# Performance work log

Hardware: AMD Instinct MI355X
Metric: run time of the kernel (lower is better)

The kernel has to match this reference:

```python
import jax, jax.numpy as jnp
import numpy as np

SEG_LENS = [2048, 8192]
DIL_RATES = [1, 2]


def _dilated_attention(q, k, v, is_causal):
    # q,k,v: [b, n, h, d]
    b, n, h, d = q.shape
    ng = len(SEG_LENS)
    g = h // ng  # heads per group (even split)
    scale = 1.0 / np.sqrt(d).astype(np.float32)
    out = jnp.zeros_like(q)
    for i, (s, r) in enumerate(zip(SEG_LENS, DIL_RATES)):
        hs = i * g
        offset = i % r  # offset_idx % dilation_rate, as in _create_dilation_pattern
        idx = np.arange(offset, s, r)  # dilated positions within a segment, length m
        m = idx.shape[0]
        ns = n // s  # number of segments
        # reshape to segments then gather dilated positions: [b, ns, m, g, d]
        qg = q[:, :, hs:hs + g, :].reshape(b, ns, s, g, d)[:, :, idx]
        kg = k[:, :, hs:hs + g, :].reshape(b, ns, s, g, d)[:, :, idx]
        vg = v[:, :, hs:hs + g, :].reshape(b, ns, s, g, d)[:, :, idx]
        # segment-local attention over dilated tokens only (structured sparsity)
        scores = jnp.einsum('bsqhd,bskhd->bshqk', qg, kg) * scale
        if is_causal:
            cm = np.tril(np.ones((m, m), dtype=bool))  # idx is sorted -> causal in dilated order
            scores = jnp.where(cm, scores, -jnp.inf)
        attn = jax.nn.softmax(scores, axis=-1)
        og = jnp.einsum('bshqk,bskhd->bsqhd', attn, vg)  # [b, ns, m, g, d]
        # scatter back to full segment positions; non-dilated positions stay zero
        full = jnp.zeros((b, ns, s, g, d), q.dtype).at[:, :, idx].set(og)
        out = out.at[:, :, hs:hs + g, :].set(full.reshape(b, n, g, d))
    return out


def setup_inputs() -> dict:
    key = jax.random.key(0)
    k1, k2, k3 = jax.random.split(key, 3)
    shape = (1, 8192, 8, 64)
    q = jax.random.normal(k1, shape, dtype=jnp.float32)
    k = jax.random.normal(k2, shape, dtype=jnp.float32)
    v = jax.random.normal(k3, shape, dtype=jnp.float32)
    return {"q": q, "k": k, "v": v, "is_causal": 1}


def reference(q, k, v, is_causal):
    return _dilated_attention(q, k, v, bool(is_causal))
```

## Files before the change

kernel.cpp:

```cpp
#include <hip/hip_runtime.h>


#define LP 72

typedef __attribute__((ext_vector_type(8))) short bf16x8;
typedef __attribute__((ext_vector_type(4))) float f32x4;
typedef const unsigned int __attribute__((address_space(1)))* gp1;
typedef unsigned int __attribute__((address_space(3)))* lp3;

__device__ __forceinline__ unsigned short f2bf(float f) {
  unsigned u = __builtin_bit_cast(unsigned, f);
  u += 0x7fff + ((u >> 16) & 1);
  return (unsigned short)(u >> 16);
}

__device__ __forceinline__ int region_base(int head) {
  return (head < 4) ? head * 524288 : 2097152 + (head - 4) * 262144;
}

__device__ __forceinline__ void gl_lds16(const unsigned short* g, unsigned short* l) {
  __builtin_amdgcn_global_load_lds((gp1)g, (lp3)l, 16, 0, 0);
}

__global__ __launch_bounds__(256, 4)
void prep_kernel(const float* __restrict__ K, const float* __restrict__ V,
                 unsigned short* __restrict__ Kb, unsigned short* __restrict__ Vt) {
  __shared__ unsigned short sT[64][LP];
  const int bid = blockIdx.x;
  int head, pos0, rate, off;
  if (bid < 512) { head = bid >> 7; pos0 = (bid & 127) * 64; rate = 1; off = 0; }
  else { int b = bid - 512; head = 4 + (b >> 6); pos0 = (b & 63) * 64; rate = 2; off = 1; }
  const int rb = region_base(head);
  const int tid = threadIdx.x;
  const int row = tid >> 2, dg = tid & 3;
  const long tok = (long)(pos0 + row) * rate + off;

  {
    const float* kp = K + tok * 512 + head * 64 + dg * 16;
    unsigned short tmp[16];
    #pragma unroll
    for (int i = 0; i < 4; ++i) {
      float4 f = ((const float4*)kp)[i];
      tmp[i * 4 + 0] = f2bf(f.x); tmp[i * 4 + 1] = f2bf(f.y);
      tmp[i * 4 + 2] = f2bf(f.z); tmp[i * 4 + 3] = f2bf(f.w);
    }
    const int s = row & 7;
    unsigned short* dstrow = Kb + rb + (long)(pos0 + row) * 64;
    *(int4*)(dstrow + (((2 * dg)     ^ s) * 8)) = ((int4*)tmp)[0];
    *(int4*)(dstrow + (((2 * dg + 1) ^ s) * 8)) = ((int4*)tmp)[1];
  }

  {
    const float* vp = V + tok * 512 + head * 64 + dg * 16;
    #pragma unroll
    for (int i = 0; i < 4; ++i) {
      float4 f = ((const float4*)vp)[i];
      unsigned* p = (unsigned*)&sT[row][dg * 16 + i * 4];
      p[0] = (unsigned)f2bf(f.x) | ((unsigned)f2bf(f.y) << 16);
      p[1] = (unsigned)f2bf(f.z) | ((unsigned)f2bf(f.w) << 16);
    }
  }
  __syncthreads();

  {
    const int wv = tid >> 6, lane = tid & 63;
    unsigned pk[8];
    #pragma unroll
    for (int j = 0; j < 8; ++j) {
      unsigned lo = sT[wv * 16 + 2 * j][lane];
      unsigned hi = sT[wv * 16 + 2 * j + 1][lane];
      pk[j] = lo | (hi << 16);
    }
    const int s = lane & 7;
    unsigned short* dstrow = Vt + rb + (long)pos0 * 64 + lane * 64;
    int4 a = {(int)pk[0], (int)pk[1], (int)pk[2], (int)pk[3]};
    int4 b = {(int)pk[4], (int)pk[5], (int)pk[6], (int)pk[7]};
    *(int4*)(dstrow + (((2 * wv)     ^ s) * 8)) = a;
    *(int4*)(dstrow + (((2 * wv + 1) ^ s) * 8)) = b;
  }
}

__global__ __launch_bounds__(256, 2)
void attn_kernel(const float* __restrict__ Q, const unsigned short* __restrict__ Kb,
                 const unsigned short* __restrict__ Vt, const int* __restrict__ IC,
                 float* __restrict__ O, float* __restrict__ Slots) {
  __shared__ __attribute__((aligned(16))) unsigned short sK[2][4096];
  __shared__ __attribute__((aligned(16))) unsigned short sV[2][4096];
  __shared__ __attribute__((aligned(16))) unsigned short sP[4][1024];

  const int bid = blockIdx.x;
  int head, q0, seg0, mseg, rate, off, grp, chunk, slot;
  if (bid < 512) {
    int h4 = bid & 3;
    int u = bid >> 2;
    chunk = u >> 6;
    int t = 63 - (u & 63);
    head = 4 + h4; seg0 = 0; mseg = 4096;
    rate = 2; off = 1; grp = 1;
    q0 = t * 64;
    slot = (h4 * 64 + t) * 2 + chunk;
  } else {
    int cc = bid - 512;
    int job = (cc & 7) | ((cc >> 8) << 3);
    int tloc = (cc & 255) >> 3;
    head = job & 3;
    seg0 = (job >> 2) * 2048;
    q0 = seg0 + tloc * 64; mseg = 2048;
    rate = 1; off = 0; grp = 0; chunk = 0; slot = 0;
  }
  const int rb = region_base(head);
  const bool causal = (*IC) != 0;
  const int tid = threadIdx.x, wave = tid >> 6, lane = tid & 63;
  const int l16 = lane & 15, quad = lane >> 4;
  const int ch0 = ((quad ^ (l16 & 7)) * 8);
  const int ch1 = ch0 ^ 32;

  const int qloc = q0 - seg0;
  const int diagkb = qloc >> 6;
  const int nkb = causal ? diagkb + 1 : (mseg >> 6);
  const int klo = grp ? chunk * 32 : 0;
  const int khi = grp ? min(nkb, klo + 32) : nkb;
  if (klo >= khi) return;

  const float QSCALE = 0.18033688011112042f;
  bf16x8 aQ[2];
  {
    long tok = (long)(q0 + wave * 16 + l16) * rate + off;
    const float* qp = Q + tok * 512 + head * 64 + quad * 8;
    #pragma unroll
    for (int kc = 0; kc < 2; ++kc) {
      float4 f0 = ((const float4*)(qp + kc * 32))[0];
      float4 f1 = ((const float4*)(qp + kc * 32))[1];
      bf16x8 a;
      a[0] = (short)f2bf(f0.x * QSCALE); a[1] = (short)f2bf(f0.y * QSCALE);
      a[2] = (short)f2bf(f0.z * QSCALE); a[3] = (short)f2bf(f0.w * QSCALE);
      a[4] = (short)f2bf(f1.x * QSCALE); a[5] = (short)f2bf(f1.y * QSCALE);
      a[6] = (short)f2bf(f1.z * QSCALE); a[7] = (short)f2bf(f1.w * QSCALE);
      aQ[kc] = a;
    }
  }

  f32x4 oacc[4], lacc;
  lacc = (f32x4){0.f, 0.f, 0.f, 0.f};
  #pragma unroll
  for (int dt = 0; dt < 4; ++dt) oacc[dt] = (f32x4){0.f, 0.f, 0.f, 0.f};
  bf16x8 vones;
  #pragma unroll
  for (int i = 0; i < 8; ++i) vones[i] = (short)0x3F80;

  unsigned short* myP = &sP[wave][0];
  const unsigned short* Ksrc = Kb + rb + (long)seg0 * 64;
  const unsigned short* Vsrc = Vt + rb + (long)seg0 * 64;

  const int o0 = wave * 1024;
  const int lo = lane * 8;
  {
    const unsigned short* kt = Ksrc + (long)klo * 4096;
    const unsigned short* vt = Vsrc + (long)klo * 4096;
    gl_lds16(kt + o0 + lo,       &sK[0][o0]);
    gl_lds16(kt + o0 + 512 + lo, &sK[0][o0 + 512]);
    gl_lds16(vt + o0 + lo,       &sV[0][o0]);
    gl_lds16(vt + o0 + 512 + lo, &sV[0][o0 + 512]);
  }

  for (int kb = klo; kb < khi; ++kb) {
    const int cur = (kb - klo) & 1;
    __syncthreads();
    if (kb + 1 < khi) {
      const unsigned short* kt = Ksrc + (long)(kb + 1) * 4096;
      const unsigned short* vt = Vsrc + (long)(kb + 1) * 4096;
      gl_lds16(kt + o0 + lo,       &sK[cur ^ 1][o0]);
      gl_lds16(kt + o0 + 512 + lo, &sK[cur ^ 1][o0 + 512]);
      gl_lds16(vt + o0 + lo,       &sV[cur ^ 1][o0]);
      gl_lds16(vt + o0 + 512 + lo, &sV[cur ^ 1][o0 + 512]);
    }
    const unsigned short* kbuf = &sK[cur][0];
    const unsigned short* vbuf = &sV[cur][0];

    f32x4 sc[4];
    #pragma unroll
    for (int c = 0; c < 4; ++c) {
      const unsigned short* krow = &kbuf[(c * 16 + l16) * 64];
      bf16x8 b0 = *(const bf16x8*)(krow + ch0);
      bf16x8 b1 = *(const bf16x8*)(krow + ch1);
      f32x4 z = (f32x4){0.f, 0.f, 0.f, 0.f};
      z = __builtin_amdgcn_mfma_f32_16x16x32_bf16(aQ[0], b0, z, 0, 0, 0);
      z = __builtin_amdgcn_mfma_f32_16x16x32_bf16(aQ[1], b1, z, 0, 0, 0);
      sc[c] = z;
    }

    const bool needMask = causal && (kb == diagkb);
    #pragma unroll
    for (int c = 0; c < 4; ++c) {
      #pragma unroll
      for (int r = 0; r < 4; ++r) {
        float e = __builtin_amdgcn_exp2f(sc[c][r]);
        if (needMask && (kb * 64 + c * 16 + l16 > qloc + wave * 16 + quad * 4 + r)) e = 0.f;
        const int qrow = quad * 4 + r;
        const int cidx = c * 2 + (l16 >> 3);
        myP[qrow * 64 + ((cidx ^ (qrow & 7)) << 3) + (l16 & 7)] = f2bf(e);
      }
    }
    const int swr = l16 & 7;
    bf16x8 aP0 = *(const bf16x8*)&myP[l16 * 64 + ((quad ^ swr) << 3)];
    bf16x8 aP1 = *(const bf16x8*)&myP[l16 * 64 + (((quad + 4) ^ swr) << 3)];
    lacc = __builtin_amdgcn_mfma_f32_16x16x32_bf16(aP0, vones, lacc, 0, 0, 0);
    lacc = __builtin_amdgcn_mfma_f32_16x16x32_bf16(aP1, vones, lacc, 0, 0, 0);

    #pragma unroll
    for (int dt = 0; dt < 4; ++dt) {
      const unsigned short* vrow = &vbuf[(dt * 16 + l16) * 64];
      bf16x8 v0 = *(const bf16x8*)(vrow + ch0);
      bf16x8 v1 = *(const bf16x8*)(vrow + ch1);
      oacc[dt] = __builtin_amdgcn_mfma_f32_16x16x32_bf16(aP0, v0, oacc[dt], 0, 0, 0);
      oacc[dt] = __builtin_amdgcn_mfma_f32_16x16x32_bf16(aP1, v1, oacc[dt], 0, 0, 0);
    }
  }

  if (grp == 1) {
    float* S = Slots + (long)slot * 4160;
    #pragma unroll
    for (int r = 0; r < 4; ++r) {
      int row = wave * 16 + quad * 4 + r;
      #pragma unroll
      for (int dt = 0; dt < 4; ++dt)
        S[row * 64 + dt * 16 + l16] = oacc[dt][r];
    }
    if (l16 == 0) {
      #pragma unroll
      for (int r = 0; r < 4; ++r)
        S[4096 + wave * 16 + quad * 4 + r] = lacc[r];
    }
  } else {
    #pragma unroll
    for (int r = 0; r < 4; ++r) {
      int tq = q0 + wave * 16 + quad * 4 + r;
      long tok = (long)tq * rate + off;
      float inv = 1.0f / lacc[r];
      float* dst = O + tok * 512 + head * 64 + l16;
      #pragma unroll
      for (int dt = 0; dt < 4; ++dt)
        dst[dt * 16] = oacc[dt][r] * inv;
    }
  }
}

__global__ __launch_bounds__(256, 4)
void combine_kernel(const float* __restrict__ Slots, const int* __restrict__ IC,
                    float* __restrict__ O) {
  const int b = blockIdx.x;
  const int h4 = b >> 6, t = b & 63;
  const bool causal = (*IC) != 0;
  const int nkb = causal ? t + 1 : 64;
  const int nc = (nkb > 32) ? 2 : 1;
  const float* s0 = Slots + (long)((h4 * 64 + t) * 2) * 4160;
  const int tid = threadIdx.x;
  const int row = tid >> 2, dq = (tid & 3) * 16;

  float4 acc[4];
  const float4* p0 = (const float4*)(s0 + row * 64 + dq);
  #pragma unroll
  for (int i = 0; i < 4; ++i) acc[i] = p0[i];
  float l = s0[4096 + row];
  if (nc == 2) {
    const float* s1 = s0 + 4160;
    const float4* p1 = (const float4*)(s1 + row * 64 + dq);
    #pragma unroll
    for (int i = 0; i < 4; ++i) {
      float4 v = p1[i];
      acc[i].x += v.x; acc[i].y += v.y; acc[i].z += v.z; acc[i].w += v.w;
    }
    l += s1[4096 + row];
  }
  const float inv = 1.0f / l;
  const long tok = (long)(t * 64 + row) * 2 + 1;
  float* dst = O + tok * 512 + (4 + h4) * 64 + dq;
  #pragma unroll
  for (int i = 0; i < 4; ++i) {
    float4 o = {acc[i].x * inv, acc[i].y * inv, acc[i].z * inv, acc[i].w * inv};
    ((float4*)dst)[i] = o;
  }
  float* dste = O + (tok - 1) * 512 + (4 + h4) * 64 + dq;
  const float4 z = {0.f, 0.f, 0.f, 0.f};
  #pragma unroll
  for (int i = 0; i < 4; ++i) ((float4*)dste)[i] = z;
}

extern "C" void kernel_launch(void* const* d_in, const int* in_sizes, int n_in,
                              void* d_out, int out_size, void* d_ws, size_t ws_size,
                              hipStream_t stream) {
  const float* q = (const float*)d_in[0];
  const float* k = (const float*)d_in[1];
  const float* v = (const float*)d_in[2];
  const int* ic = (const int*)d_in[3];
  unsigned short* Kb = (unsigned short*)d_ws;
  unsigned short* Vt = Kb + 3145728;
  float* Slots = (float*)((char*)d_ws + 12582912);
  prep_kernel<<<dim3(768), dim3(256), 0, stream>>>(k, v, Kb, Vt);
  attn_kernel<<<dim3(1024), dim3(256), 0, stream>>>(q, Kb, Vt, ic, (float*)d_out, Slots);
  combine_kernel<<<dim3(256), dim3(256), 0, stream>>>(Slots, ic, (float*)d_out);
}
```

Baseline: 138.8 us.

## Transpose MFMA operand roles to compute S^T and O^T, drop ones-MFMA row sum

Swaps the A/B operands of the QK and PV MFMAs so each lane holds a full query column, which lets the softmax denominator be a per-lane scalar sum plus two cross-lane shuffles instead of an extra pair of MFMAs against a ones vector. P is written to LDS as packed 64-bit stores instead of scalar 16-bit stores. Output and partial slots are written as float4 vectors instead of scalar floats. The row sum is now taken in fp32 before bf16 rounding, which changes numerics slightly.

```diff
diff --git a/kernel.cpp b/kernel.cpp
--- a/kernel.cpp
+++ b/kernel.cpp
@@ -123,7 +123,7 @@
   if (klo >= khi) return;
 
   const float QSCALE = 0.18033688011112042f;
-  bf16x8 aQ[2];
+  bf16x8 bQ[2];
   {
     long tok = (long)(q0 + wave * 16 + l16) * rate + off;
     const float* qp = Q + tok * 512 + head * 64 + quad * 8;
@@ -136,17 +136,14 @@
       a[2] = (short)f2bf(f0.z * QSCALE); a[3] = (short)f2bf(f0.w * QSCALE);
       a[4] = (short)f2bf(f1.x * QSCALE); a[5] = (short)f2bf(f1.y * QSCALE);
       a[6] = (short)f2bf(f1.z * QSCALE); a[7] = (short)f2bf(f1.w * QSCALE);
-      aQ[kc] = a;
-    }
-  }
-
-  f32x4 oacc[4], lacc;
-  lacc = (f32x4){0.f, 0.f, 0.f, 0.f};
+      bQ[kc] = a;
+    }
+  }
+
+  f32x4 oacc[4];
+  float lsum = 0.f;
   #pragma unroll
   for (int dt = 0; dt < 4; ++dt) oacc[dt] = (f32x4){0.f, 0.f, 0.f, 0.f};
-  bf16x8 vones;
-  #pragma unroll
-  for (int i = 0; i < 8; ++i) vones[i] = (short)0x3F80;
 
   unsigned short* myP = &sP[wave][0];
   const unsigned short* Ksrc = Kb + rb + (long)seg0 * 64;
@@ -181,66 +178,66 @@
     #pragma unroll
     for (int c = 0; c < 4; ++c) {
       const unsigned short* krow = &kbuf[(c * 16 + l16) * 64];
-      bf16x8 b0 = *(const bf16x8*)(krow + ch0);
-      bf16x8 b1 = *(const bf16x8*)(krow + ch1);
+      bf16x8 a0 = *(const bf16x8*)(krow + ch0);
+      bf16x8 a1 = *(const bf16x8*)(krow + ch1);
       f32x4 z = (f32x4){0.f, 0.f, 0.f, 0.f};
-      z = __builtin_amdgcn_mfma_f32_16x16x32_bf16(aQ[0], b0, z, 0, 0, 0);
-      z = __builtin_amdgcn_mfma_f32_16x16x32_bf16(aQ[1], b1, z, 0, 0, 0);
+      z = __builtin_amdgcn_mfma_f32_16x16x32_bf16(a0, bQ[0], z, 0, 0, 0);
+      z = __builtin_amdgcn_mfma_f32_16x16x32_bf16(a1, bQ[1], z, 0, 0, 0);
       sc[c] = z;
     }
 
     const bool needMask = causal && (kb == diagkb);
+    const int myq = qloc + wave * 16 + l16;
+    const int sw = l16 & 7;
     #pragma unroll
     for (int c = 0; c < 4; ++c) {
+      unsigned short pb[4];
       #pragma unroll
       for (int r = 0; r < 4; ++r) {
         float e = __builtin_amdgcn_exp2f(sc[c][r]);
-        if (needMask && (kb * 64 + c * 16 + l16 > qloc + wave * 16 + quad * 4 + r)) e = 0.f;
-        const int qrow = quad * 4 + r;
-        const int cidx = c * 2 + (l16 >> 3);
-        myP[qrow * 64 + ((cidx ^ (qrow & 7)) << 3) + (l16 & 7)] = f2bf(e);
+        if (needMask && (kb * 64 + c * 16 + quad * 4 + r > myq)) e = 0.f;
+        lsum += e;
+        pb[r] = f2bf(e);
       }
-    }
-    const int swr = l16 & 7;
-    bf16x8 aP0 = *(const bf16x8*)&myP[l16 * 64 + ((quad ^ swr) << 3)];
-    bf16x8 aP1 = *(const bf16x8*)&myP[l16 * 64 + (((quad + 4) ^ swr) << 3)];
-    lacc = __builtin_amdgcn_mfma_f32_16x16x32_bf16(aP0, vones, lacc, 0, 0, 0);
-    lacc = __builtin_amdgcn_mfma_f32_16x16x32_bf16(aP1, vones, lacc, 0, 0, 0);
+      unsigned w0 = (unsigned)pb[0] | ((unsigned)pb[1] << 16);
+      unsigned w1 = (unsigned)pb[2] | ((unsigned)pb[3] << 16);
+      const int wch = (c * 2 + (quad >> 1)) ^ sw;
+      *(uint2*)&myP[l16 * 64 + wch * 8 + (quad & 1) * 4] = (uint2){w0, w1};
+    }
+    bf16x8 bP0 = *(const bf16x8*)&myP[l16 * 64 + ((quad ^ sw) << 3)];
+    bf16x8 bP1 = *(const bf16x8*)&myP[l16 * 64 + (((4 + quad) ^ sw) << 3)];
 
     #pragma unroll
     for (int dt = 0; dt < 4; ++dt) {
       const unsigned short* vrow = &vbuf[(dt * 16 + l16) * 64];
       bf16x8 v0 = *(const bf16x8*)(vrow + ch0);
       bf16x8 v1 = *(const bf16x8*)(vrow + ch1);
-      oacc[dt] = __builtin_amdgcn_mfma_f32_16x16x32_bf16(aP0, v0, oacc[dt], 0, 0, 0);
-      oacc[dt] = __builtin_amdgcn_mfma_f32_16x16x32_bf16(aP1, v1, oacc[dt], 0, 0, 0);
-    }
-  }
+      oacc[dt] = __builtin_amdgcn_mfma_f32_16x16x32_bf16(v0, bP0, oacc[dt], 0, 0, 0);
+      oacc[dt] = __builtin_amdgcn_mfma_f32_16x16x32_bf16(v1, bP1, oacc[dt], 0, 0, 0);
+    }
+  }
+
+  lsum += __shfl_xor(lsum, 16);
+  lsum += __shfl_xor(lsum, 32);
+
+  const int row = wave * 16 + l16;
 
   if (grp == 1) {
     float* S = Slots + (long)slot * 4160;
     #pragma unroll
-    for (int r = 0; r < 4; ++r) {
-      int row = wave * 16 + quad * 4 + r;
-      #pragma unroll
-      for (int dt = 0; dt < 4; ++dt)
-        S[row * 64 + dt * 16 + l16] = oacc[dt][r];
-    }
-    if (l16 == 0) {
-      #pragma unroll
-      for (int r = 0; r < 4; ++r)
-        S[4096 + wave * 16 + quad * 4 + r] = lacc[r];
-    }
+    for (int dt = 0; dt < 4; ++dt)
+      *(float4*)&S[row * 64 + dt * 16 + quad * 4] =
+          (float4){oacc[dt][0], oacc[dt][1], oacc[dt][2], oacc[dt][3]};
+    if (quad == 0) S[4096 + row] = lsum;
   } else {
-    #pragma unroll
-    for (int r = 0; r < 4; ++r) {
-      int tq = q0 + wave * 16 + quad * 4 + r;
-      long tok = (long)tq * rate + off;
-      float inv = 1.0f / lacc[r];
-      float* dst = O + tok * 512 + head * 64 + l16;
-      #pragma unroll
-      for (int dt = 0; dt < 4; ++dt)
-        dst[dt * 16] = oacc[dt][r] * inv;
+    long tok = (long)(q0 + row) * rate + off;
+    float inv = 1.0f / lsum;
+    float* dst = O + tok * 512 + head * 64 + quad * 4;
+    #pragma unroll
+    for (int dt = 0; dt < 4; ++dt) {
+      float4 v = {oacc[dt][0] * inv, oacc[dt][1] * inv,
+                  oacc[dt][2] * inv, oacc[dt][3] * inv};
+      *(float4*)(dst + dt * 16) = v;
     }
   }
 }
```

Result: no change. 139.7 us (+0.6%).
